# Kernel optimization log

Hardware: AMD Instinct MI355X
Metric: run time of the kernel (lower is better)

## Reference

```python
import jax, jax.numpy as jnp
import numpy as np

DIM = 1024
HEADS = 16
DIM_HEAD = 64
INNER = HEADS * DIM_HEAD  # 1024
SCALE = DIM ** (-0.5)  # module scales by dim**-0.5 (not dim_head)


def setup_inputs() -> dict:
    key = jax.random.key(0)
    kx, kqkv, kwo, kbo = jax.random.split(key, 4)
    x = jax.random.normal(kx, (2, 2048, DIM), dtype=jnp.float32)
    W_qkv = jax.random.normal(kqkv, (DIM, 3 * INNER), dtype=jnp.float32) * (DIM ** -0.5)
    W_out = jax.random.normal(kwo, (INNER, DIM), dtype=jnp.float32) * (INNER ** -0.5)
    b_out = jax.random.normal(kbo, (DIM,), dtype=jnp.float32) * 0.01
    return {"x": x, "W_qkv": W_qkv, "W_out": W_out, "b_out": b_out}


def reference(x, W_qkv, W_out, b_out):
    b, n, _ = x.shape
    qkv = x @ W_qkv  # [b, n, 3*inner]
    q, k, v = jnp.split(qkv, 3, axis=-1)
    # [b, n, h*d] -> [b, h, n, d]
    reshape = lambda t: t.reshape(b, n, HEADS, DIM_HEAD).transpose(0, 2, 1, 3)
    q, k, v = reshape(q), reshape(k), reshape(v)
    dots = jnp.einsum('bhid,bhjd->bhij', q, k) * SCALE  # [b, h, n, n]
    attn = jax.nn.softmax(dots, axis=-1)
    out = jnp.einsum('bhij,bhjd->bhid', attn, v)  # [b, h, n, d]
    out = out.transpose(0, 2, 1, 3).reshape(b, n, INNER)
    return out @ W_out + b_out
```

## Files before the change

kernel.cpp:

```cpp
#include <hip/hip_runtime.h>

typedef __bf16 bf16x8 __attribute__((ext_vector_type(8)));
typedef __bf16 bf16x4 __attribute__((ext_vector_type(4)));
typedef float f32x4 __attribute__((ext_vector_type(4)));
typedef float f32x16 __attribute__((ext_vector_type(16)));

__device__ __forceinline__ void async16(void* lds, const void* g) {
  __builtin_amdgcn_global_load_lds(
      (__attribute__((address_space(1))) unsigned int*)(g),
      (__attribute__((address_space(3))) unsigned int*)(lds), 16, 0, 0);
}

__device__ __forceinline__ int detect_block(const unsigned short* win, int* cnt_sh) {
  if (threadIdx.x == 0) *cnt_sh = 0;
  __syncthreads();
  int c = 0;
#pragma unroll
  for (int j = 0; j < 8; j++) {
    const unsigned short u = win[threadIdx.x * 8 + j];
    if (((u >> 7) & 0xFF) >= 0xC0) c++;
  }
  if (c) atomicAdd(cnt_sh, c);
  __syncthreads();
  return (*cnt_sh >= 64) ? 1 : 0;
}

__global__ void cvt_bf16(const void* __restrict__ src, __bf16* __restrict__ dst,
                         long n, int* __restrict__ flagp) {
  __shared__ int cnt;
  const long base = (long)blockIdx.x * 2048;
  const int f = detect_block((const unsigned short*)src + base, &cnt);
  if (blockIdx.x == 0 && threadIdx.x == 0) *flagp = f;
  const long i = base + threadIdx.x * 8;
  if (i >= n) return;
  if (f) {
    const float* s = (const float*)src;
#pragma unroll
    for (int j = 0; j < 8; j++) dst[i + j] = (__bf16)s[i + j];
  } else {
    *(bf16x8*)&dst[i] = *(const bf16x8*)((const __bf16*)src + i);
  }
}

__global__ __launch_bounds__(256) void transpose_both(
    const void* __restrict__ Wqkv, const void* __restrict__ Wout,
    __bf16* __restrict__ WqkvT, __bf16* __restrict__ WoutT)
{
  __shared__ __bf16 tile[64][65];
  __shared__ int cnt;
  const int bx = blockIdx.x;
  const void* in;  __bf16* out;  int R, C, tx;
  if (bx < 48) { in = Wqkv; out = WqkvT; R = 1024; C = 3072; tx = bx; }
  else         { in = Wout; out = WoutT; R = 1024; C = 1024; tx = bx - 48; }
  const int tc = tx * 64;
  const int tr = blockIdx.y * 64;
  const int f = detect_block((const unsigned short*)in + (long)(tr * C + tc), &cnt);
  const int t = threadIdx.x;
#pragma unroll
  for (int i = 0; i < 16; i++) {
    const int idx = t + 256 * i;
    const int r = idx >> 6, c = idx & 63;
    const long g = (long)(tr + r) * C + tc + c;
    tile[r][c] = f ? (__bf16)((const float*)in)[g] : ((const __bf16*)in)[g];
  }
  __syncthreads();
#pragma unroll
  for (int i = 0; i < 16; i++) {
    const int idx = t + 256 * i;
    const int r = idx >> 6, c = idx & 63;
    out[(long)(tc + r) * R + tr + c] = tile[c][r];
  }
}

__global__ __launch_bounds__(256, 2) void gemm_qkv(
    const __bf16* __restrict__ A, const __bf16* __restrict__ Bt,
    __bf16* __restrict__ Cqk, __bf16* __restrict__ Vt)
{
  __shared__ __bf16 smem[128 * 136];
  __bf16* As = smem;
  __bf16* Bs = smem + 4096;
  const int t = threadIdx.x;
  const int l = t & 63;
  const int w = t >> 6;
  const int wr = w >> 1, wc = w & 1;
  const long m0 = (long)blockIdx.x * 128;
  const long n0 = (long)blockIdx.y * 128;
  const int K = 1024;

  const int srow = w * 16 + (l >> 2);
  const int skof = (l & 3) * 8;
  const __bf16* gA = A + (m0 + srow) * (long)K + skof;
  const __bf16* gB = Bt + (n0 + srow) * (long)K + skof;
  __bf16* lA = As + w * 512 + l * 8;
  __bf16* lB = Bs + w * 512 + l * 8;

  f32x4 acc[4][4] = {};

  for (int k0 = 0; k0 < K; k0 += 32) {
    __syncthreads();
    async16(lA,        gA);
    async16(lA + 2048, gA + 64 * (long)K);
    async16(lB,        gB);
    async16(lB + 2048, gB + 64 * (long)K);
    gA += 32; gB += 32;
    __syncthreads();

    bf16x8 af[4], bfr[4];
#pragma unroll
    for (int mi = 0; mi < 4; mi++)
      af[mi] = *(const bf16x8*)&As[(wr * 64 + mi * 16 + (l & 15)) * 32 + (l >> 4) * 8];
#pragma unroll
    for (int ni = 0; ni < 4; ni++)
      bfr[ni] = *(const bf16x8*)&Bs[(wc * 64 + ni * 16 + (l & 15)) * 32 + (l >> 4) * 8];
#pragma unroll
    for (int mi = 0; mi < 4; mi++)
#pragma unroll
      for (int ni = 0; ni < 4; ni++)
        acc[mi][ni] = __builtin_amdgcn_mfma_f32_16x16x32_bf16(af[mi], bfr[ni], acc[mi][ni], 0, 0, 0);
  }

  if (n0 < 2048) {
#pragma unroll
    for (int mi = 0; mi < 4; mi++)
#pragma unroll
      for (int ni = 0; ni < 4; ni++) {
        const long col = n0 + wc * 64 + ni * 16 + (l & 15);
#pragma unroll
        for (int r = 0; r < 4; r++) {
          const long row = m0 + wr * 64 + mi * 16 + (l >> 4) * 4 + r;
          Cqk[row * 2048 + col] = (__bf16)acc[mi][ni][r];
        }
      }
  } else {
    __syncthreads();
#pragma unroll
    for (int mi = 0; mi < 4; mi++)
#pragma unroll
      for (int ni = 0; ni < 4; ni++) {
        const int c = wc * 64 + ni * 16 + (l & 15);
        const int r = wr * 64 + mi * 16 + (l >> 4) * 4;
        bf16x4 pk;
#pragma unroll
        for (int k = 0; k < 4; k++) pk[k] = (__bf16)acc[mi][ni][k];
        *(bf16x4*)&smem[c * 136 + r] = pk;
      }
    __syncthreads();
    const int b = (int)(m0 >> 11);
    const int nbase = (int)(m0 & 2047);
#pragma unroll
    for (int i = 0; i < 8; i++) {
      const int c = (t >> 4) + i * 16;
      const int r8 = (t & 15) * 8;
      const bf16x8 v = *(const bf16x8*)&smem[c * 136 + r8];
      const int vcol = (int)(n0 - 2048) + c;
      *(bf16x8*)&Vt[((long)(b * 16 + (vcol >> 6)) * 64 + (vcol & 63)) * 2048 + nbase + r8] = v;
    }
  }
}

__global__ __launch_bounds__(256, 2) void gemm_out(
    const __bf16* __restrict__ A, const __bf16* __restrict__ Bt,
    const void* __restrict__ bias_raw, void* __restrict__ C,
    const int* __restrict__ flagp)
{
  __shared__ __bf16 As[128 * 32];
  __shared__ __bf16 Bs[64 * 32];
  const int t = threadIdx.x;
  const int l = t & 63;
  const int w = t >> 6;
  const int wr = w >> 1, wc = w & 1;
  const long m0 = (long)blockIdx.x * 128;
  const long n0 = (long)blockIdx.y * 64;
  const int of = *flagp;
  const int K = 1024;

  const int srow = w * 16 + (l >> 2);
  const int skof = (l & 3) * 8;
  const __bf16* gA = A + (m0 + srow) * (long)K + skof;
  const __bf16* gB = Bt + (n0 + srow) * (long)K + skof;
  __bf16* lA = As + w * 512 + l * 8;
  __bf16* lB = Bs + w * 512 + l * 8;

  f32x4 acc[4][2] = {};

  for (int k0 = 0; k0 < K; k0 += 32) {
    __syncthreads();
    async16(lA,        gA);
    async16(lA + 2048, gA + 64 * (long)K);
    async16(lB,        gB);
    gA += 32; gB += 32;
    __syncthreads();

    bf16x8 af[4], bfr[2];
#pragma unroll
    for (int mi = 0; mi < 4; mi++)
      af[mi] = *(const bf16x8*)&As[(wr * 64 + mi * 16 + (l & 15)) * 32 + (l >> 4) * 8];
#pragma unroll
    for (int ni = 0; ni < 2; ni++)
      bfr[ni] = *(const bf16x8*)&Bs[(wc * 32 + ni * 16 + (l & 15)) * 32 + (l >> 4) * 8];
#pragma unroll
    for (int mi = 0; mi < 4; mi++)
#pragma unroll
      for (int ni = 0; ni < 2; ni++)
        acc[mi][ni] = __builtin_amdgcn_mfma_f32_16x16x32_bf16(af[mi], bfr[ni], acc[mi][ni], 0, 0, 0);
  }

#pragma unroll
  for (int mi = 0; mi < 4; mi++)
#pragma unroll
    for (int ni = 0; ni < 2; ni++) {
      const long col = n0 + wc * 32 + ni * 16 + (l & 15);
      const float bv = of ? ((const float*)bias_raw)[col]
                          : (float)((const __bf16*)bias_raw)[col];
#pragma unroll
      for (int r = 0; r < 4; r++) {
        const long row = m0 + wr * 64 + mi * 16 + (l >> 4) * 4 + r;
        const float val = acc[mi][ni][r] + bv;
        const long off = row * 1024 + col;
        if (of) ((float*)C)[off] = val;
        else    ((__bf16*)C)[off] = (__bf16)val;
      }
    }
}

#define EXP2_SCALE 0.045084439f

__global__ __launch_bounds__(256, 4) void attn_kernel(
    const __bf16* __restrict__ qk, const __bf16* __restrict__ Vt,
    __bf16* __restrict__ O)
{
  __shared__ __bf16 Qs[64 * 64];
  __shared__ __bf16 Ks[64 * 64];
  __shared__ __bf16 Vts[64 * 64];
  __shared__ __bf16 Ps[64 * 64];

  const int t = threadIdx.x;
  const int l = t & 63;
  const int w = t >> 6;
  const int wi = w & 1, wj = w >> 1;
  const int qt = blockIdx.x;
  const int bh = blockIdx.y;
  const int b = bh >> 4, h = bh & 15;
  const long q_row0 = (long)b * 2048 + qt * 64;

  const int srow = w * 8 + (l >> 3);
  const int sdof = ((l & 7) ^ (l >> 3)) * 8;

  {
    const __bf16* g = qk + (q_row0 + srow) * 2048 + h * 64 + sdof;
    __bf16* lp = Qs + w * 512 + l * 8;
    async16(lp,        g);
    async16(lp + 2048, g + (long)32 * 2048);
  }

  const __bf16* gK = qk + ((long)b * 2048 + srow) * 2048 + 1024 + h * 64 + sdof;
  const __bf16* gV = Vt + ((long)bh * 64 + srow) * 2048 + sdof;
  __bf16* lK = Ks + w * 512 + l * 8;
  __bf16* lV = Vts + w * 512 + l * 8;

  __syncthreads();

  const int i7 = l & 7;
  bf16x8 qf[4];
#pragma unroll
  for (int kc = 0; kc < 4; kc++)
    qf[kc] = *(const bf16x8*)&Qs[(wi * 32 + (l & 31)) * 64 + (((kc * 2 + (l >> 5)) ^ i7) * 8)];

  f32x16 acc_o = {0,0,0,0,0,0,0,0,0,0,0,0,0,0,0,0};
  float l_i = 0.0f;

  for (int j0 = 0; j0 < 2048; j0 += 64) {
    __syncthreads();
    async16(lK,        gK);
    async16(lK + 2048, gK + 32 * 2048);
    async16(lV,        gV);
    async16(lV + 2048, gV + 32 * 2048);
    gK += (long)64 * 2048;
    gV += 64;
    __syncthreads();

    f32x16 st = {0,0,0,0,0,0,0,0,0,0,0,0,0,0,0,0};
#pragma unroll
    for (int kc = 0; kc < 4; kc++) {
      const int swz = ((kc * 2 + (l >> 5)) ^ i7) * 8;
      const bf16x8 ak = *(const bf16x8*)&Ks[(wj * 32 + (l & 31)) * 64 + swz];
      st = __builtin_amdgcn_mfma_f32_32x32x16_bf16(ak, qf[kc], st, 0, 0, 0);
    }

    float rs = 0.0f;
#pragma unroll
    for (int r = 0; r < 16; r++) {
      const float p = exp2f(st[r] * EXP2_SCALE);
      st[r] = p;
      rs += p;
    }
    rs += __shfl_xor(rs, 32, 64);
    l_i += rs;

    {
      const int ibase = (wi * 32 + (l & 31)) * 64;
      const int sub = 4 * (l >> 5);
#pragma unroll
      for (int q = 0; q < 4; q++) {
        bf16x4 pk;
#pragma unroll
        for (int r = 0; r < 4; r++) pk[r] = (__bf16)st[q * 4 + r];
        const int gj = 4 * wj + q;
        *(bf16x4*)&Ps[ibase + ((gj ^ i7) * 8) + sub] = pk;
      }
    }
    __syncthreads();

#pragma unroll
    for (int kc = 0; kc < 4; kc++) {
      const int swz = ((kc * 2 + (l >> 5)) ^ i7) * 8;
      const bf16x8 ap = *(const bf16x8*)&Ps[(wi * 32 + (l & 31)) * 64 + swz];
      const bf16x8 bv = *(const bf16x8*)&Vts[(wj * 32 + (l & 31)) * 64 + swz];
      acc_o = __builtin_amdgcn_mfma_f32_32x32x16_bf16(ap, bv, acc_o, 0, 0, 0);
    }
  }

  __syncthreads();
  float* lbuf = (float*)Ps;
  if (l < 32) lbuf[w * 32 + l] = l_i;
  __syncthreads();
#pragma unroll
  for (int r = 0; r < 16; r++) {
    const int i_loc = (r & 3) + 8 * (r >> 2) + 4 * (l >> 5);
    const float lsum = lbuf[wi * 32 + i_loc] + lbuf[(wi + 2) * 32 + i_loc];
    const long row = q_row0 + wi * 32 + i_loc;
    const long col = (long)h * 64 + wj * 32 + (l & 31);
    O[row * 1024 + col] = (__bf16)(acc_o[r] / lsum);
  }
}

extern "C" void kernel_launch(void* const* d_in, const int* in_sizes, int n_in,
                              void* d_out, int out_size, void* d_ws, size_t ws_size,
                              hipStream_t stream) {
  const void* x    = d_in[0];
  const void* Wqkv = d_in[1];
  const void* Wout = d_in[2];
  const void* bout = d_in[3];

  char* ws = (char*)d_ws;
  int*    flagp = (int*)ws;
  __bf16* xb    = (__bf16*)(ws + 4096);
  __bf16* WqkvT = (__bf16*)(ws + 4096 +  8388608);
  __bf16* WoutT = (__bf16*)(ws + 4096 + 14680064);
  __bf16* qkbuf = (__bf16*)(ws + 4096 + 16777216);
  __bf16* VtBuf = (__bf16*)(ws + 4096 + 33554432);
  __bf16* Obuf  = (__bf16*)(ws + 4096 + 41943040);

  hipLaunchKernelGGL(cvt_bf16, dim3(2048), dim3(256), 0, stream,
                     x, xb, (long)4194304, flagp);
  hipLaunchKernelGGL(transpose_both, dim3(64, 16), dim3(256), 0, stream,
                     Wqkv, Wout, WqkvT, WoutT);
  hipLaunchKernelGGL(gemm_qkv, dim3(32, 24), dim3(256), 0, stream,
                     xb, WqkvT, qkbuf, VtBuf);
  hipLaunchKernelGGL(attn_kernel, dim3(32, 32), dim3(256), 0, stream,
                     qkbuf, VtBuf, Obuf);
  hipLaunchKernelGGL(gemm_out, dim3(32, 16), dim3(256), 0, stream,
                     Obuf, WoutT, bout, d_out, flagp);
}
```

Measured before the change: 207.2 us.

## Double-buffer GEMM and attention loads, fuse prep kernels, keep P in registers

New measurement: 212.9 us. 2.7% more time.

```diff
diff --git a/kernel.cpp b/kernel.cpp
--- a/kernel.cpp
+++ b/kernel.cpp
@@ -25,60 +25,62 @@
   return (*cnt_sh >= 64) ? 1 : 0;
 }
 
-__global__ void cvt_bf16(const void* __restrict__ src, __bf16* __restrict__ dst,
-                         long n, int* __restrict__ flagp) {
-  __shared__ int cnt;
-  const long base = (long)blockIdx.x * 2048;
-  const int f = detect_block((const unsigned short*)src + base, &cnt);
-  if (blockIdx.x == 0 && threadIdx.x == 0) *flagp = f;
-  const long i = base + threadIdx.x * 8;
-  if (i >= n) return;
-  if (f) {
-    const float* s = (const float*)src;
-#pragma unroll
-    for (int j = 0; j < 8; j++) dst[i + j] = (__bf16)s[i + j];
-  } else {
-    *(bf16x8*)&dst[i] = *(const bf16x8*)((const __bf16*)src + i);
-  }
-}
-
-__global__ __launch_bounds__(256) void transpose_both(
-    const void* __restrict__ Wqkv, const void* __restrict__ Wout,
-    __bf16* __restrict__ WqkvT, __bf16* __restrict__ WoutT)
+__global__ __launch_bounds__(256) void prep(
+    const void* __restrict__ x, const void* __restrict__ Wqkv,
+    const void* __restrict__ Wout, __bf16* __restrict__ xb,
+    __bf16* __restrict__ WqkvT, __bf16* __restrict__ WoutT,
+    int* __restrict__ flagp)
 {
-  __shared__ __bf16 tile[64][65];
+  __shared__ __bf16 tile[64 * 65];
   __shared__ int cnt;
   const int bx = blockIdx.x;
-  const void* in;  __bf16* out;  int R, C, tx;
-  if (bx < 48) { in = Wqkv; out = WqkvT; R = 1024; C = 3072; tx = bx; }
-  else         { in = Wout; out = WoutT; R = 1024; C = 1024; tx = bx - 48; }
-  const int tc = tx * 64;
-  const int tr = blockIdx.y * 64;
-  const int f = detect_block((const unsigned short*)in + (long)(tr * C + tc), &cnt);
   const int t = threadIdx.x;
+
+  if (bx < 2048) {
+    const long base = (long)bx * 2048;
+    const int f = detect_block((const unsigned short*)x + base, &cnt);
+    if (bx == 0 && t == 0) *flagp = f;
+    const long i = base + t * 8;
+    if (f) {
+      const float* s = (const float*)x;
+#pragma unroll
+      for (int j = 0; j < 8; j++) xb[i + j] = (__bf16)s[i + j];
+    } else {
+      *(bf16x8*)&xb[i] = *(const bf16x8*)((const __bf16*)x + i);
+    }
+    return;
+  }
+
+  const void* in;  __bf16* out;  int R = 1024, C, tcx, tr;
+  if (bx < 2816) {
+    const int idx = bx - 2048;
+    in = Wqkv; out = WqkvT; C = 3072; tcx = (idx % 48) * 64; tr = (idx / 48) * 64;
+  } else {
+    const int idx = bx - 2816;
+    in = Wout; out = WoutT; C = 1024; tcx = (idx % 16) * 64; tr = (idx / 16) * 64;
+  }
+  const int f = detect_block((const unsigned short*)in + (long)tr * C + tcx, &cnt);
 #pragma unroll
   for (int i = 0; i < 16; i++) {
     const int idx = t + 256 * i;
     const int r = idx >> 6, c = idx & 63;
-    const long g = (long)(tr + r) * C + tc + c;
-    tile[r][c] = f ? (__bf16)((const float*)in)[g] : ((const __bf16*)in)[g];
+    const long g = (long)(tr + r) * C + tcx + c;
+    tile[r * 65 + c] = f ? (__bf16)((const float*)in)[g] : ((const __bf16*)in)[g];
   }
   __syncthreads();
 #pragma unroll
   for (int i = 0; i < 16; i++) {
     const int idx = t + 256 * i;
     const int r = idx >> 6, c = idx & 63;
-    out[(long)(tc + r) * R + tr + c] = tile[c][r];
-  }
-}
-
-__global__ __launch_bounds__(256, 2) void gemm_qkv(
+    out[(long)(tcx + r) * R + tr + c] = tile[c * 65 + r];
+  }
+}
+
+__global__ __launch_bounds__(256, 3) void gemm_qkv(
     const __bf16* __restrict__ A, const __bf16* __restrict__ Bt,
     __bf16* __restrict__ Cqk, __bf16* __restrict__ Vt)
 {
-  __shared__ __bf16 smem[128 * 136];
-  __bf16* As = smem;
-  __bf16* Bs = smem + 4096;
+  __shared__ __bf16 smem[17408];
   const int t = threadIdx.x;
   const int l = t & 63;
   const int w = t >> 6;
@@ -91,20 +93,29 @@
   const int skof = (l & 3) * 8;
   const __bf16* gA = A + (m0 + srow) * (long)K + skof;
   const __bf16* gB = Bt + (n0 + srow) * (long)K + skof;
-  __bf16* lA = As + w * 512 + l * 8;
-  __bf16* lB = Bs + w * 512 + l * 8;
+  const int Ao[2] = {0, 8192}, Bo[2] = {4096, 12288};
+  const int lof = w * 512 + l * 8;
+
+  async16(smem + Ao[0] + lof,        gA);
+  async16(smem + Ao[0] + 2048 + lof, gA + 64 * (long)K);
+  async16(smem + Bo[0] + lof,        gB);
+  async16(smem + Bo[0] + 2048 + lof, gB + 64 * (long)K);
+  gA += 32; gB += 32;
+  __syncthreads();
 
   f32x4 acc[4][4] = {};
 
-  for (int k0 = 0; k0 < K; k0 += 32) {
-    __syncthreads();
-    async16(lA,        gA);
-    async16(lA + 2048, gA + 64 * (long)K);
-    async16(lB,        gB);
-    async16(lB + 2048, gB + 64 * (long)K);
-    gA += 32; gB += 32;
-    __syncthreads();
-
+  for (int it = 0; it < 32; it++) {
+    if (it < 31) {
+      const int nb = (it + 1) & 1;
+      async16(smem + Ao[nb] + lof,        gA);
+      async16(smem + Ao[nb] + 2048 + lof, gA + 64 * (long)K);
+      async16(smem + Bo[nb] + lof,        gB);
+      async16(smem + Bo[nb] + 2048 + lof, gB + 64 * (long)K);
+      gA += 32; gB += 32;
+    }
+    const __bf16* As = smem + Ao[it & 1];
+    const __bf16* Bs = smem + Bo[it & 1];
     bf16x8 af[4], bfr[4];
 #pragma unroll
     for (int mi = 0; mi < 4; mi++)
@@ -117,6 +128,7 @@
 #pragma unroll
       for (int ni = 0; ni < 4; ni++)
         acc[mi][ni] = __builtin_amdgcn_mfma_f32_16x16x32_bf16(af[mi], bfr[ni], acc[mi][ni], 0, 0, 0);
+    __syncthreads();
   }
 
   if (n0 < 2048) {
@@ -132,7 +144,6 @@
         }
       }
   } else {
-    __syncthreads();
 #pragma unroll
     for (int mi = 0; mi < 4; mi++)
 #pragma unroll
@@ -163,8 +174,7 @@
     const void* __restrict__ bias_raw, void* __restrict__ C,
     const int* __restrict__ flagp)
 {
-  __shared__ __bf16 As[128 * 32];
-  __shared__ __bf16 Bs[64 * 32];
+  __shared__ __bf16 smem[12288];
   const int t = threadIdx.x;
   const int l = t & 63;
   const int w = t >> 6;
@@ -178,19 +188,27 @@
   const int skof = (l & 3) * 8;
   const __bf16* gA = A + (m0 + srow) * (long)K + skof;
   const __bf16* gB = Bt + (n0 + srow) * (long)K + skof;
-  __bf16* lA = As + w * 512 + l * 8;
-  __bf16* lB = Bs + w * 512 + l * 8;
+  const int Ao[2] = {0, 6144}, Bo[2] = {4096, 10240};
+  const int lof = w * 512 + l * 8;
+
+  async16(smem + Ao[0] + lof,        gA);
+  async16(smem + Ao[0] + 2048 + lof, gA + 64 * (long)K);
+  async16(smem + Bo[0] + lof,        gB);
+  gA += 32; gB += 32;
+  __syncthreads();
 
   f32x4 acc[4][2] = {};
 
-  for (int k0 = 0; k0 < K; k0 += 32) {
-    __syncthreads();
-    async16(lA,        gA);
-    async16(lA + 2048, gA + 64 * (long)K);
-    async16(lB,        gB);
-    gA += 32; gB += 32;
-    __syncthreads();
-
+  for (int it = 0; it < 32; it++) {
+    if (it < 31) {
+      const int nb = (it + 1) & 1;
+      async16(smem + Ao[nb] + lof,        gA);
+      async16(smem + Ao[nb] + 2048 + lof, gA + 64 * (long)K);
+      async16(smem + Bo[nb] + lof,        gB);
+      gA += 32; gB += 32;
+    }
+    const __bf16* As = smem + Ao[it & 1];
+    const __bf16* Bs = smem + Bo[it & 1];
     bf16x8 af[4], bfr[2];
 #pragma unroll
     for (int mi = 0; mi < 4; mi++)
@@ -203,6 +221,7 @@
 #pragma unroll
       for (int ni = 0; ni < 2; ni++)
         acc[mi][ni] = __builtin_amdgcn_mfma_f32_16x16x32_bf16(af[mi], bfr[ni], acc[mi][ni], 0, 0, 0);
+    __syncthreads();
   }
 
 #pragma unroll
@@ -229,61 +248,63 @@
     const __bf16* __restrict__ qk, const __bf16* __restrict__ Vt,
     __bf16* __restrict__ O)
 {
-  __shared__ __bf16 Qs[64 * 64];
-  __shared__ __bf16 Ks[64 * 64];
-  __shared__ __bf16 Vts[64 * 64];
-  __shared__ __bf16 Ps[64 * 64];
-
+  __shared__ __bf16 smem[20480];
   const int t = threadIdx.x;
   const int l = t & 63;
   const int w = t >> 6;
   const int wi = w & 1, wj = w >> 1;
+  const int hl = l >> 5;
+  const int i7 = l & 7;
   const int qt = blockIdx.x;
   const int bh = blockIdx.y;
-  const int b = bh >> 4, h = bh & 15;
+  const int b = bh >> 4, head = bh & 15;
   const long q_row0 = (long)b * 2048 + qt * 64;
 
   const int srow = w * 8 + (l >> 3);
   const int sdof = ((l & 7) ^ (l >> 3)) * 8;
+  const int lof = w * 512 + l * 8;
+  const int Ko[2] = {4096, 12288}, Vo[2] = {8192, 16384};
 
   {
-    const __bf16* g = qk + (q_row0 + srow) * 2048 + h * 64 + sdof;
-    __bf16* lp = Qs + w * 512 + l * 8;
-    async16(lp,        g);
-    async16(lp + 2048, g + (long)32 * 2048);
-  }
-
-  const __bf16* gK = qk + ((long)b * 2048 + srow) * 2048 + 1024 + h * 64 + sdof;
+    const __bf16* g = qk + (q_row0 + srow) * 2048 + head * 64 + sdof;
+    async16(smem + lof,        g);
+    async16(smem + 2048 + lof, g + (long)32 * 2048);
+  }
+  const __bf16* gK = qk + ((long)b * 2048 + srow) * 2048 + 1024 + head * 64 + sdof;
   const __bf16* gV = Vt + ((long)bh * 64 + srow) * 2048 + sdof;
-  __bf16* lK = Ks + w * 512 + l * 8;
-  __bf16* lV = Vts + w * 512 + l * 8;
-
-  __syncthreads();
-
-  const int i7 = l & 7;
+  async16(smem + Ko[0] + lof,        gK);
+  async16(smem + Ko[0] + 2048 + lof, gK + 32 * 2048);
+  async16(smem + Vo[0] + lof,        gV);
+  async16(smem + Vo[0] + 2048 + lof, gV + 32 * 2048);
+  gK += (long)64 * 2048;
+  gV += 64;
+  __syncthreads();
+
   bf16x8 qf[4];
 #pragma unroll
   for (int kc = 0; kc < 4; kc++)
-    qf[kc] = *(const bf16x8*)&Qs[(wi * 32 + (l & 31)) * 64 + (((kc * 2 + (l >> 5)) ^ i7) * 8)];
-
-  f32x16 acc_o = {0,0,0,0,0,0,0,0,0,0,0,0,0,0,0,0};
+    qf[kc] = *(const bf16x8*)&smem[(wi * 32 + (l & 31)) * 64 + (((kc * 2 + hl) ^ i7) * 8)];
+
+  f32x16 acc[2] = {};
   float l_i = 0.0f;
 
-  for (int j0 = 0; j0 < 2048; j0 += 64) {
-    __syncthreads();
-    async16(lK,        gK);
-    async16(lK + 2048, gK + 32 * 2048);
-    async16(lV,        gV);
-    async16(lV + 2048, gV + 32 * 2048);
-    gK += (long)64 * 2048;
-    gV += 64;
-    __syncthreads();
+  for (int it = 0; it < 32; it++) {
+    if (it < 31) {
+      const int nb = (it + 1) & 1;
+      async16(smem + Ko[nb] + lof,        gK);
+      async16(smem + Ko[nb] + 2048 + lof, gK + 32 * 2048);
+      async16(smem + Vo[nb] + lof,        gV);
+      async16(smem + Vo[nb] + 2048 + lof, gV + 32 * 2048);
+      gK += (long)64 * 2048;
+      gV += 64;
+    }
+    const __bf16* Ks = smem + Ko[it & 1];
+    const __bf16* Vs = smem + Vo[it & 1];
 
     f32x16 st = {0,0,0,0,0,0,0,0,0,0,0,0,0,0,0,0};
 #pragma unroll
     for (int kc = 0; kc < 4; kc++) {
-      const int swz = ((kc * 2 + (l >> 5)) ^ i7) * 8;
-      const bf16x8 ak = *(const bf16x8*)&Ks[(wj * 32 + (l & 31)) * 64 + swz];
+      const bf16x8 ak = *(const bf16x8*)&Ks[(wj * 32 + (l & 31)) * 64 + (((kc * 2 + hl) ^ i7) * 8)];
       st = __builtin_amdgcn_mfma_f32_32x32x16_bf16(ak, qf[kc], st, 0, 0, 0);
     }
 
@@ -297,40 +318,57 @@
     rs += __shfl_xor(rs, 32, 64);
     l_i += rs;
 
-    {
-      const int ibase = (wi * 32 + (l & 31)) * 64;
-      const int sub = 4 * (l >> 5);
-#pragma unroll
-      for (int q = 0; q < 4; q++) {
-        bf16x4 pk;
-#pragma unroll
-        for (int r = 0; r < 4; r++) pk[r] = (__bf16)st[q * 4 + r];
-        const int gj = 4 * wj + q;
-        *(bf16x4*)&Ps[ibase + ((gj ^ i7) * 8) + sub] = pk;
+    unsigned pw[8], qw[8];
+#pragma unroll
+    for (int k2 = 0; k2 < 8; k2++) {
+      union { __bf16 h2[2]; unsigned u; } cv;
+      cv.h2[0] = (__bf16)st[2 * k2];
+      cv.h2[1] = (__bf16)st[2 * k2 + 1];
+      pw[k2] = cv.u;
+    }
+#pragma unroll
+    for (int k2 = 0; k2 < 8; k2++)
+      qw[k2] = (unsigned)__shfl_xor((int)pw[k2], 32, 64);
+
+#pragma unroll
+    for (int m = 0; m < 2; m++) {
+      union { unsigned u[4]; bf16x8 v; } fa;
+      fa.u[0] = hl ? qw[4 * m + 2] : pw[4 * m + 0];
+      fa.u[1] = hl ? qw[4 * m + 3] : pw[4 * m + 1];
+      fa.u[2] = hl ? pw[4 * m + 2] : qw[4 * m + 0];
+      fa.u[3] = hl ? pw[4 * m + 3] : qw[4 * m + 1];
+#pragma unroll
+      for (int nd = 0; nd < 2; nd++) {
+        const bf16x8 bv = *(const bf16x8*)&Vs[(nd * 32 + (l & 31)) * 64 + (((4 * wj + 2 * m + hl) ^ i7) * 8)];
+        acc[nd] = __builtin_amdgcn_mfma_f32_32x32x16_bf16(fa.v, bv, acc[nd], 0, 0, 0);
       }
     }
     __syncthreads();
-
-#pragma unroll
-    for (int kc = 0; kc < 4; kc++) {
-      const int swz = ((kc * 2 + (l >> 5)) ^ i7) * 8;
-      const bf16x8 ap = *(const bf16x8*)&Ps[(wi * 32 + (l & 31)) * 64 + swz];
-      const bf16x8 bv = *(const bf16x8*)&Vts[(wj * 32 + (l & 31)) * 64 + swz];
-      acc_o = __builtin_amdgcn_mfma_f32_32x32x16_bf16(ap, bv, acc_o, 0, 0, 0);
-    }
-  }
-
-  __syncthreads();
-  float* lbuf = (float*)Ps;
-  if (l < 32) lbuf[w * 32 + l] = l_i;
-  __syncthreads();
-#pragma unroll
-  for (int r = 0; r < 16; r++) {
-    const int i_loc = (r & 3) + 8 * (r >> 2) + 4 * (l >> 5);
-    const float lsum = lbuf[wi * 32 + i_loc] + lbuf[(wi + 2) * 32 + i_loc];
-    const long row = q_row0 + wi * 32 + i_loc;
-    const long col = (long)h * 64 + wj * 32 + (l & 31);
-    O[row * 1024 + col] = (__bf16)(acc_o[r] / lsum);
+  }
+
+  float* sc = (float*)(smem + 4096);
+  float* lb = (float*)(smem + 12288);
+  if (l < 32) lb[w * 32 + l] = l_i;
+  if (wj == 1) {
+#pragma unroll
+    for (int nd = 0; nd < 2; nd++)
+#pragma unroll
+      for (int r = 0; r < 16; r++)
+        sc[wi * 2048 + nd * 1024 + (int)l * 16 + r] = acc[nd][r];
+  }
+  __syncthreads();
+  if (wj == 0) {
+#pragma unroll
+    for (int r = 0; r < 16; r++) {
+      const int iloc = (r & 3) + 8 * (r >> 2) + 4 * hl;
+      const float lt = lb[wi * 32 + iloc] + lb[(wi + 2) * 32 + iloc];
+      const long row = q_row0 + wi * 32 + iloc;
+#pragma unroll
+      for (int nd = 0; nd < 2; nd++) {
+        const float o = acc[nd][r] + sc[wi * 2048 + nd * 1024 + (int)l * 16 + r];
+        O[row * 1024 + head * 64 + nd * 32 + (l & 31)] = (__bf16)(o / lt);
+      }
+    }
   }
 }
 
@@ -351,10 +389,8 @@
   __bf16* VtBuf = (__bf16*)(ws + 4096 + 33554432);
   __bf16* Obuf  = (__bf16*)(ws + 4096 + 41943040);
 
-  hipLaunchKernelGGL(cvt_bf16, dim3(2048), dim3(256), 0, stream,
-                     x, xb, (long)4194304, flagp);
-  hipLaunchKernelGGL(transpose_both, dim3(64, 16), dim3(256), 0, stream,
-                     Wqkv, Wout, WqkvT, WoutT);
+  hipLaunchKernelGGL(prep, dim3(3072), dim3(256), 0, stream,
+                     x, Wqkv, Wout, xb, WqkvT, WoutT, flagp);
   hipLaunchKernelGGL(gemm_qkv, dim3(32, 24), dim3(256), 0, stream,
                      xb, WqkvT, qkbuf, VtBuf);
   hipLaunchKernelGGL(attn_kernel, dim3(32, 32), dim3(256), 0, stream,
```
